# Kernel optimization log

Measured on AMD Instinct MI355X. Metric: run time of the kernel, lower is better.

The kernel has to match this reference:

```python
import jax, jax.numpy as jnp
import numpy as np

B, S, HID = 1, 2048, 2048
H, KVH, D, VD = 32, 8, 128, 128
R = 64  # rope_dim = head_dim * partial_rotary_factor, rounded down to even
N_REP = H // KVH
SCALE = D ** -0.5
NEG = -1e9


def _rotate_half(x):
    half = x.shape[-1] // 2
    return jnp.concatenate([-x[..., half:], x[..., :half]], axis=-1)


def setup_inputs() -> dict:
    key = jax.random.key(0)
    ks = jax.random.split(key, 8)
    hidden_states = jax.random.normal(ks[0], (B, S, HID), dtype=jnp.float32)
    # RoPE angles: standard inverse-frequency positional embedding of width R
    inv_freq = 1.0 / (10000.0 ** (np.arange(0, R, 2, dtype=np.float32) / R))
    pos = np.arange(S, dtype=np.float32)
    freqs = np.outer(pos, inv_freq)                       # [S, R/2]
    emb = np.concatenate([freqs, freqs], axis=-1)         # [S, R]
    cos = jnp.asarray(np.cos(emb))[None].repeat(B, axis=0)  # [B, S, R]
    sin = jnp.asarray(np.sin(emb))[None].repeat(B, axis=0)
    # additive causal mask [B, 1, S, S]
    causal = jnp.triu(jnp.full((S, S), NEG, dtype=jnp.float32), k=1)
    attention_mask = jnp.broadcast_to(causal[None, None], (B, 1, S, S))
    std = 0.02
    Wq = jax.random.normal(ks[1], (H * D, HID), dtype=jnp.float32) * std
    Wk = jax.random.normal(ks[2], (KVH * D, HID), dtype=jnp.float32) * std
    Wv = jax.random.normal(ks[3], (KVH * VD, HID), dtype=jnp.float32) * std
    Wo = jax.random.normal(ks[4], (HID, H * VD), dtype=jnp.float32) * std
    sink_bias = jax.random.normal(ks[5], (H,), dtype=jnp.float32) * 0.5
    return {"hidden_states": hidden_states, "cos": cos, "sin": sin,
            "attention_mask": attention_mask, "Wq": Wq, "Wk": Wk, "Wv": Wv,
            "Wo": Wo, "sink_bias": sink_bias}


def reference(hidden_states, cos, sin, attention_mask, Wq, Wk, Wv, Wo, sink_bias):
    b, s, _ = hidden_states.shape
    # projections -> [B, heads, S, dim]
    q = (hidden_states @ Wq.T).reshape(b, s, H, D).transpose(0, 2, 1, 3)
    k = (hidden_states @ Wk.T).reshape(b, s, KVH, D).transpose(0, 2, 1, 3)
    v = (hidden_states @ Wv.T).reshape(b, s, KVH, VD).transpose(0, 2, 1, 3)
    # partial RoPE on first R dims
    c = cos[:, None, :, :]  # [B,1,S,R]
    si = sin[:, None, :, :]
    q_r, q_n = q[..., :R], q[..., R:]
    k_r, k_n = k[..., :R], k[..., R:]
    q = jnp.concatenate([q_r * c + _rotate_half(q_r) * si, q_n], axis=-1)
    k = jnp.concatenate([k_r * c + _rotate_half(k_r) * si, k_n], axis=-1)
    # GQA: repeat kv heads
    k_rep = jnp.repeat(k, N_REP, axis=1)
    v_rep = jnp.repeat(v, N_REP, axis=1)
    scores = jnp.einsum('bhqd,bhkd->bhqk', q, k_rep) * SCALE + attention_mask
    # extra attention-sink logit column per head
    sinks = jnp.broadcast_to(sink_bias.reshape(1, H, 1, 1), (b, H, s, 1))
    aw = jnp.concatenate([scores, sinks], axis=-1)            # [B,H,S,S+1]
    probs = jax.nn.softmax(aw, axis=-1)[..., :-1]             # drop sink column
    out = jnp.einsum('bhqk,bhkd->bhqd', probs, v_rep)
    out = out.transpose(0, 2, 1, 3).reshape(b, s, H * VD)
    return out @ Wo.T
```

## Files before the change

kernel.cpp:

```cpp
#include <hip/hip_runtime.h>

typedef unsigned short u16;
typedef unsigned int   u32;
typedef __bf16  bf16x8 __attribute__((ext_vector_type(8)));
typedef float   f32x4  __attribute__((ext_vector_type(4)));
typedef u16     u16x4  __attribute__((ext_vector_type(4)));
typedef u16     u16x8  __attribute__((ext_vector_type(8)));

#define S_LEN 2048
#define NH 32
#define NKVH 8
#define HD 128
#define QKVST 6144
#define AOST  4096
#define ATT_SCALE 0.08838834764831845f
#define RESCALE_THR 8.0f

__device__ __forceinline__ u16 f2bf(float f){
  u32 u = __builtin_bit_cast(u32, f);
  u += 0x7FFFu + ((u >> 16) & 1u);
  return (u16)(u >> 16);
}
__device__ __forceinline__ float bf2f(u16 h){
  u32 u = ((u32)h) << 16;
  return __builtin_bit_cast(float, u);
}
__device__ __forceinline__ void gload_lds16(const u16* g, u16* l){
  __builtin_amdgcn_global_load_lds(
      (const __attribute__((address_space(1))) void*)g,
      (__attribute__((address_space(3))) void*)l, 16, 0, 0);
}

__global__ void cvt_kernel(const f32x4* __restrict__ in, u16x4* __restrict__ out, int n4){
  int i = blockIdx.x * 256 + threadIdx.x;
  if (i >= n4) return;
  f32x4 v = in[i];
  u16x4 o;
  o[0] = f2bf(v[0]); o[1] = f2bf(v[1]); o[2] = f2bf(v[2]); o[3] = f2bf(v[3]);
  out[i] = o;
}

template<int OUT_BF16, int ROPE>
__global__ __launch_bounds__(256, 2)
void gemm_bt_kernel(const u16* __restrict__ X, const u16* __restrict__ W,
                    void* __restrict__ Cv, int M, int N, int K,
                    const float* __restrict__ cosv, const float* __restrict__ sinv){
  __shared__ __align__(16) u16 As[2][2][128 * 32];
  __shared__ __align__(16) u16 Bs[2][2][128 * 32];
  const int m0 = blockIdx.y * 128, n0 = blockIdx.x * 128;
  const int tid = threadIdx.x;
  const int wave = tid >> 6, lane = tid & 63;
  const int wm = wave >> 1, wn = wave & 1;
  const int g = lane >> 4, ln = lane & 15;
  const int r0 = tid >> 2;
  const int cc = (tid & 3) * 8;
  f32x4 acc[4][4] = {};
  const u16* xa0 = X + (size_t)(m0 + r0) * K + cc;
  const u16* xa1 = X + (size_t)(m0 + r0 + 64) * K + cc;
  const u16* wb0 = W + (size_t)(n0 + r0) * K + cc;
  const u16* wb1 = W + (size_t)(n0 + r0 + 64) * K + cc;

  auto stage = [&](int buf, int k0){
    #pragma unroll
    for (int s = 0; s < 2; s++){
      const int kc = k0 + s * 32;
      gload_lds16(xa0 + kc, &As[buf][s][tid * 8]);
      gload_lds16(xa1 + kc, &As[buf][s][2048 + tid * 8]);
      gload_lds16(wb0 + kc, &Bs[buf][s][tid * 8]);
      gload_lds16(wb1 + kc, &Bs[buf][s][2048 + tid * 8]);
    }
  };

  stage(0, 0);
  __syncthreads();
  int cur = 0;
  for (int k0 = 0; k0 < K; k0 += 64){
    if (k0 + 64 < K) stage(cur ^ 1, k0 + 64);
    #pragma unroll
    for (int s = 0; s < 2; s++){
      bf16x8 a[4], b[4];
      #pragma unroll
      for (int f = 0; f < 4; f++) a[f] = *(const bf16x8*)&As[cur][s][(wm * 64 + f * 16 + ln) * 32 + g * 8];
      #pragma unroll
      for (int f = 0; f < 4; f++) b[f] = *(const bf16x8*)&Bs[cur][s][(wn * 64 + f * 16 + ln) * 32 + g * 8];
      __builtin_amdgcn_s_setprio(1);
      #pragma unroll
      for (int i = 0; i < 4; i++)
        #pragma unroll
        for (int j = 0; j < 4; j++)
          acc[i][j] = __builtin_amdgcn_mfma_f32_16x16x32_bf16(a[i], b[j], acc[i][j], 0, 0, 0);
      __builtin_amdgcn_s_setprio(0);
    }
    __syncthreads();
    cur ^= 1;
  }
  if (ROPE && wn == 0 && n0 < 5120){
    #pragma unroll
    for (int i = 0; i < 4; i++)
      #pragma unroll
      for (int r = 0; r < 4; r++){
        const int row = m0 + wm * 64 + i * 16 + g * 4 + r;
        #pragma unroll
        for (int j = 0; j < 2; j++){
          const int d = j * 16 + ln;
          float c  = cosv[row * 64 + d];
          float sn = sinv[row * 64 + d];
          float x0 = acc[i][j][r], x1 = acc[i][j + 2][r];
          acc[i][j][r]     = x0 * c - x1 * sn;
          acc[i][j + 2][r] = x1 * c + x0 * sn;
        }
      }
  }
  #pragma unroll
  for (int i = 0; i < 4; i++)
    #pragma unroll
    for (int j = 0; j < 4; j++)
      #pragma unroll
      for (int r = 0; r < 4; r++){
        int row = m0 + wm * 64 + i * 16 + g * 4 + r;
        int col = n0 + wn * 64 + j * 16 + ln;
        if (OUT_BF16) ((u16*)Cv)[(size_t)row * N + col] = f2bf(acc[i][j][r]);
        else          ((float*)Cv)[(size_t)row * N + col] = acc[i][j][r];
      }
}

__global__ void vtrans_kernel(const u16* __restrict__ QKV, u16* __restrict__ VT){
  int idx = blockIdx.x * 256 + threadIdx.x;
  if (idx >= NKVH * HD * S_LEN) return;
  int s   = idx & (S_LEN - 1);
  int vd  = (idx >> 11) & (HD - 1);
  int kvh = idx >> 18;
  VT[idx] = QKV[(size_t)s * QKVST + 5120 + kvh * HD + vd];
}

__global__ __launch_bounds__(256, 2)
void attn_kernel(const u16* __restrict__ QKV, const u16* __restrict__ VT,
                 const float* __restrict__ sinkb, u16* __restrict__ AO){
  __shared__ __align__(16) u16 Ks[2][64 * 128];
  __shared__ __align__(16) u16 Vs[2][144 * 64];
  __shared__ __align__(16) u16 Ps[4][16 * 64];
  const int b   = blockIdx.x;
  const int kvh = b & 7;
  const int h   = kvh * 4 + ((b >> 3) & 3);
  const int qt  = 31 - (b >> 5);
  const int tid = threadIdx.x;
  const int w = tid >> 6, lane = tid & 63;
  const int g = lane >> 4, ln = lane & 15;
  const int q0 = qt * 64;
  const int qw = q0 + w * 16;

  const u16* Kbase = QKV + 4096 + kvh * HD;
  const u16* Vbase = VT + (size_t)kvh * HD * S_LEN;

  auto stage = [&](int buf, int kt){
    const int k0 = kt * 64;
    #pragma unroll
    for (int p = 0; p < 4; p++){
      int idx = p * 256 + tid;
      int r = idx >> 4, c16 = idx & 15;
      gload_lds16(Kbase + (size_t)(k0 + r) * QKVST + ((c16 ^ (r & 7)) * 8), &Ks[buf][idx * 8]);
    }
    #pragma unroll
    for (int p = 0; p < 4; p++){
      int idx = p * 256 + tid;
      int vd = idx >> 3, c8 = idx & 7;
      gload_lds16(Vbase + (size_t)vd * S_LEN + k0 + ((c8 ^ (vd & 7)) * 8), &Vs[buf][idx * 8]);
    }
  };

  for (int i = tid; i < 16 * 64; i += 256){
    u16 v = (i < 64) ? (u16)0x3F80 : (u16)0;
    Vs[0][128 * 64 + i] = v;
    Vs[1][128 * 64 + i] = v;
  }

  bf16x8 qf[4];
  const u16* qrow = QKV + (size_t)(qw + ln) * QKVST + h * HD;
  #pragma unroll
  for (int t = 0; t < 4; t++) qf[t] = *(const bf16x8*)(qrow + t * 32 + g * 8);

  f32x4 O[9] = {};
  float m_r[4];
  #pragma unroll
  for (int r = 0; r < 4; r++) m_r[r] = -3.0e38f;

  const int nkt = qt + 1;
  stage(0, 0);
  __syncthreads();
  int cur = 0;

  for (int kt = 0; kt < nkt; kt++){
    const int k0 = kt * 64;
    if (kt + 1 < nkt) stage(cur ^ 1, kt + 1);

    const u16* Kc = Ks[cur];
    f32x4 sc[4] = {};
    __builtin_amdgcn_s_setprio(1);
    #pragma unroll
    for (int f = 0; f < 4; f++){
      const int krow = f * 16 + ln;
      #pragma unroll
      for (int t = 0; t < 4; t++){
        bf16x8 kf = *(const bf16x8*)&Kc[krow * 128 + ((t * 32 + g * 8) ^ ((ln & 7) << 3))];
        sc[f] = __builtin_amdgcn_mfma_f32_16x16x32_bf16(qf[t], kf, sc[f], 0, 0, 0);
      }
    }
    __builtin_amdgcn_s_setprio(0);

    const bool diag = (kt == qt);
    float pv[4][4];
    #pragma unroll
    for (int f = 0; f < 4; f++)
      #pragma unroll
      for (int r = 0; r < 4; r++){
        float v = sc[f][r] * ATT_SCALE;
        if (diag && (k0 + f * 16 + ln > qw + g * 4 + r)) v = -1e30f;
        pv[f][r] = v;
      }
    float mx[4];
    #pragma unroll
    for (int r = 0; r < 4; r++){
      float t = fmaxf(fmaxf(pv[0][r], pv[1][r]), fmaxf(pv[2][r], pv[3][r]));
      #pragma unroll
      for (int d = 1; d < 16; d <<= 1) t = fmaxf(t, __shfl_xor(t, d));
      mx[r] = t;
    }
    int ok = (mx[0] <= m_r[0] + RESCALE_THR) & (mx[1] <= m_r[1] + RESCALE_THR)
           & (mx[2] <= m_r[2] + RESCALE_THR) & (mx[3] <= m_r[3] + RESCALE_THR);
    if (!__all(ok)){
      float sf_[4];
      #pragma unroll
      for (int r = 0; r < 4; r++){
        float mn = fmaxf(m_r[r], mx[r]);
        sf_[r] = __expf(m_r[r] - mn);
        m_r[r] = mn;
      }
      #pragma unroll
      for (int fn = 0; fn < 9; fn++)
        #pragma unroll
        for (int r = 0; r < 4; r++) O[fn][r] *= sf_[r];
    }
    u16* Pw = Ps[w];
    #pragma unroll
    for (int r = 0; r < 4; r++){
      const int row = g * 4 + r;
      #pragma unroll
      for (int f = 0; f < 4; f++){
        float p = __expf(pv[f][r] - m_r[r]);
        Pw[row * 64 + ((f * 16 + ln) ^ ((row & 7) << 3))] = f2bf(p);
      }
    }
    const u16* Vc = Vs[cur];
    bf16x8 pa0 = *(const bf16x8*)&Pw[ln * 64 + ((g * 8)      ^ ((ln & 7) << 3))];
    bf16x8 pa1 = *(const bf16x8*)&Pw[ln * 64 + ((32 + g * 8) ^ ((ln & 7) << 3))];
    __builtin_amdgcn_s_setprio(1);
    #pragma unroll
    for (int fn = 0; fn < 9; fn++){
      const int vr = fn * 16 + ln;
      bf16x8 v0 = *(const bf16x8*)&Vc[vr * 64 + ((g * 8)      ^ ((ln & 7) << 3))];
      bf16x8 v1 = *(const bf16x8*)&Vc[vr * 64 + ((32 + g * 8) ^ ((ln & 7) << 3))];
      O[fn] = __builtin_amdgcn_mfma_f32_16x16x32_bf16(pa0, v0, O[fn], 0, 0, 0);
      O[fn] = __builtin_amdgcn_mfma_f32_16x16x32_bf16(pa1, v1, O[fn], 0, 0, 0);
    }
    __builtin_amdgcn_s_setprio(0);

    __syncthreads();
    cur ^= 1;
  }
  float sb = sinkb[h];
  #pragma unroll
  for (int r = 0; r < 4; r++){
    float l = __shfl(O[8][r], lane & 48);
    float mt = fmaxf(m_r[r], sb);
    float lt = l * __expf(m_r[r] - mt) + __expf(sb - mt);
    float osc = __expf(m_r[r] - mt) / lt;
    #pragma unroll
    for (int fn = 0; fn < 8; fn++)
      AO[(size_t)(qw + g * 4 + r) * AOST + h * HD + fn * 16 + ln] = f2bf(O[fn][r] * osc);
  }
}

extern "C" void kernel_launch(void* const* d_in, const int* in_sizes, int n_in,
                              void* d_out, int out_size, void* d_ws, size_t ws_size,
                              hipStream_t stream){
  (void)in_sizes; (void)n_in; (void)out_size; (void)ws_size;
  const float* hs    = (const float*)d_in[0];
  const float* cosv  = (const float*)d_in[1];
  const float* sinv  = (const float*)d_in[2];
  const float* Wq    = (const float*)d_in[4];
  const float* Wk    = (const float*)d_in[5];
  const float* Wv    = (const float*)d_in[6];
  const float* Wo    = (const float*)d_in[7];
  const float* sinkb = (const float*)d_in[8];
  float* out = (float*)d_out;

  char* ws = (char*)d_ws;
  u16* XB    = (u16*)(ws);
  u16* WQKVB = (u16*)(ws + 8388608);
  u16* WOB   = (u16*)(ws + 33554432);
  u16* QKV   = (u16*)(ws + 50331648);
  u16* VT    = (u16*)(ws + 75497472);
  u16* AO    = (u16*)(ws + 79691776);

  cvt_kernel<<<4096, 256, 0, stream>>>((const f32x4*)hs, (u16x4*)XB, 1048576);
  cvt_kernel<<<8192, 256, 0, stream>>>((const f32x4*)Wq, (u16x4*)WQKVB, 2097152);
  cvt_kernel<<<2048, 256, 0, stream>>>((const f32x4*)Wk, (u16x4*)(WQKVB + 4096 * 2048), 524288);
  cvt_kernel<<<2048, 256, 0, stream>>>((const f32x4*)Wv, (u16x4*)(WQKVB + 5120 * 2048), 524288);
  cvt_kernel<<<8192, 256, 0, stream>>>((const f32x4*)Wo, (u16x4*)WOB, 2097152);

  gemm_bt_kernel<1, 1><<<dim3(48, 16), 256, 0, stream>>>(XB, WQKVB, QKV, 2048, 6144, 2048, cosv, sinv);

  vtrans_kernel<<<8192, 256, 0, stream>>>(QKV, VT);

  attn_kernel<<<dim3(1024), 256, 0, stream>>>(QKV, VT, sinkb, AO);

  gemm_bt_kernel<0, 0><<<dim3(16, 16), 256, 0, stream>>>(AO, WOB, out, 2048, 2048, 4096, nullptr, nullptr);
}
```

Measured before the change: 259.3 us.

## Double attention Q tile per block and fold softmax scale into QKV GEMM

```diff
diff --git a/kernel.cpp b/kernel.cpp
--- a/kernel.cpp
+++ b/kernel.cpp
@@ -94,22 +94,32 @@
     __syncthreads();
     cur ^= 1;
   }
-  if (ROPE && wn == 0 && n0 < 5120){
-    #pragma unroll
-    for (int i = 0; i < 4; i++)
-      #pragma unroll
-      for (int r = 0; r < 4; r++){
-        const int row = m0 + wm * 64 + i * 16 + g * 4 + r;
-        #pragma unroll
-        for (int j = 0; j < 2; j++){
-          const int d = j * 16 + ln;
-          float c  = cosv[row * 64 + d];
-          float sn = sinv[row * 64 + d];
-          float x0 = acc[i][j][r], x1 = acc[i][j + 2][r];
-          acc[i][j][r]     = x0 * c - x1 * sn;
-          acc[i][j + 2][r] = x1 * c + x0 * sn;
-        }
-      }
+  if (ROPE){
+    if (wn == 0 && n0 < 5120){
+      #pragma unroll
+      for (int i = 0; i < 4; i++)
+        #pragma unroll
+        for (int r = 0; r < 4; r++){
+          const int row = m0 + wm * 64 + i * 16 + g * 4 + r;
+          #pragma unroll
+          for (int j = 0; j < 2; j++){
+            const int d = j * 16 + ln;
+            float c  = cosv[row * 64 + d];
+            float sn = sinv[row * 64 + d];
+            float x0 = acc[i][j][r], x1 = acc[i][j + 2][r];
+            acc[i][j][r]     = x0 * c - x1 * sn;
+            acc[i][j + 2][r] = x1 * c + x0 * sn;
+          }
+        }
+    }
+    if (n0 < 4096){
+      #pragma unroll
+      for (int i = 0; i < 4; i++)
+        #pragma unroll
+        for (int j = 0; j < 4; j++)
+          #pragma unroll
+          for (int r = 0; r < 4; r++) acc[i][j][r] *= ATT_SCALE;
+    }
   }
   #pragma unroll
   for (int i = 0; i < 4; i++)
@@ -137,17 +147,17 @@
 void attn_kernel(const u16* __restrict__ QKV, const u16* __restrict__ VT,
                  const float* __restrict__ sinkb, u16* __restrict__ AO){
   __shared__ __align__(16) u16 Ks[2][64 * 128];
-  __shared__ __align__(16) u16 Vs[2][144 * 64];
-  __shared__ __align__(16) u16 Ps[4][16 * 64];
+  __shared__ __align__(16) u16 Vs[2][128 * 64];
+  __shared__ __align__(16) u16 Ps[4][32 * 64];
   const int b   = blockIdx.x;
   const int kvh = b & 7;
   const int h   = kvh * 4 + ((b >> 3) & 3);
-  const int qt  = 31 - (b >> 5);
+  const int qt  = 15 - (b >> 5);
   const int tid = threadIdx.x;
   const int w = tid >> 6, lane = tid & 63;
   const int g = lane >> 4, ln = lane & 15;
-  const int q0 = qt * 64;
-  const int qw = q0 + w * 16;
+  const int q0 = qt * 128;
+  const int qw = q0 + w * 32;
 
   const u16* Kbase = QKV + 4096 + kvh * HD;
   const u16* Vbase = VT + (size_t)kvh * HD * S_LEN;
@@ -168,23 +178,28 @@
     }
   };
 
-  for (int i = tid; i < 16 * 64; i += 256){
-    u16 v = (i < 64) ? (u16)0x3F80 : (u16)0;
-    Vs[0][128 * 64 + i] = v;
-    Vs[1][128 * 64 + i] = v;
+  u16x8 ob;
+  #pragma unroll
+  for (int j = 0; j < 8; j++) ob[j] = (ln == 0) ? (u16)0x3F80 : (u16)0;
+  const bf16x8 onesf = __builtin_bit_cast(bf16x8, ob);
+
+  bf16x8 qf[2][4];
+  #pragma unroll
+  for (int qh = 0; qh < 2; qh++){
+    const u16* qrow = QKV + (size_t)(qw + qh * 16 + ln) * QKVST + h * HD;
+    #pragma unroll
+    for (int t = 0; t < 4; t++) qf[qh][t] = *(const bf16x8*)(qrow + t * 32 + g * 8);
   }
 
-  bf16x8 qf[4];
-  const u16* qrow = QKV + (size_t)(qw + ln) * QKVST + h * HD;
-  #pragma unroll
-  for (int t = 0; t < 4; t++) qf[t] = *(const bf16x8*)(qrow + t * 32 + g * 8);
-
-  f32x4 O[9] = {};
-  float m_r[4];
-  #pragma unroll
-  for (int r = 0; r < 4; r++) m_r[r] = -3.0e38f;
-
-  const int nkt = qt + 1;
+  f32x4 O[2][8] = {};
+  f32x4 L[2] = {};
+  float m_r[2][4];
+  #pragma unroll
+  for (int qh = 0; qh < 2; qh++)
+    #pragma unroll
+    for (int r = 0; r < 4; r++) m_r[qh][r] = -3.0e38f;
+
+  const int nkt = 2 * qt + 2;
   stage(0, 0);
   __syncthreads();
   int cur = 0;
@@ -193,91 +208,121 @@
     const int k0 = kt * 64;
     if (kt + 1 < nkt) stage(cur ^ 1, kt + 1);
 
-    const u16* Kc = Ks[cur];
-    f32x4 sc[4] = {};
-    __builtin_amdgcn_s_setprio(1);
-    #pragma unroll
-    for (int f = 0; f < 4; f++){
-      const int krow = f * 16 + ln;
-      #pragma unroll
-      for (int t = 0; t < 4; t++){
-        bf16x8 kf = *(const bf16x8*)&Kc[krow * 128 + ((t * 32 + g * 8) ^ ((ln & 7) << 3))];
-        sc[f] = __builtin_amdgcn_mfma_f32_16x16x32_bf16(qf[t], kf, sc[f], 0, 0, 0);
+    if (k0 < qw + 32){
+      const u16* Kc = Ks[cur];
+      f32x4 sc[2][4] = {};
+      __builtin_amdgcn_s_setprio(1);
+      #pragma unroll
+      for (int f = 0; f < 4; f++){
+        const int krow = f * 16 + ln;
+        #pragma unroll
+        for (int t = 0; t < 4; t++){
+          bf16x8 kf = *(const bf16x8*)&Kc[krow * 128 + ((t * 32 + g * 8) ^ ((ln & 7) << 3))];
+          sc[0][f] = __builtin_amdgcn_mfma_f32_16x16x32_bf16(qf[0][t], kf, sc[0][f], 0, 0, 0);
+          sc[1][f] = __builtin_amdgcn_mfma_f32_16x16x32_bf16(qf[1][t], kf, sc[1][f], 0, 0, 0);
+        }
       }
-    }
-    __builtin_amdgcn_s_setprio(0);
-
-    const bool diag = (kt == qt);
-    float pv[4][4];
-    #pragma unroll
-    for (int f = 0; f < 4; f++)
-      #pragma unroll
-      for (int r = 0; r < 4; r++){
-        float v = sc[f][r] * ATT_SCALE;
-        if (diag && (k0 + f * 16 + ln > qw + g * 4 + r)) v = -1e30f;
-        pv[f][r] = v;
+      __builtin_amdgcn_s_setprio(0);
+
+      const bool needmask = (k0 + 63 > qw);
+      float pv[2][4][4];
+      #pragma unroll
+      for (int qh = 0; qh < 2; qh++)
+        #pragma unroll
+        for (int f = 0; f < 4; f++)
+          #pragma unroll
+          for (int r = 0; r < 4; r++){
+            float v = sc[qh][f][r];
+            if (needmask && (k0 + f * 16 + ln > qw + qh * 16 + g * 4 + r)) v = -1e30f;
+            pv[qh][f][r] = v;
+          }
+      float mx[2][4];
+      #pragma unroll
+      for (int qh = 0; qh < 2; qh++)
+        #pragma unroll
+        for (int r = 0; r < 4; r++){
+          float t = fmaxf(fmaxf(pv[qh][0][r], pv[qh][1][r]), fmaxf(pv[qh][2][r], pv[qh][3][r]));
+          #pragma unroll
+          for (int d = 1; d < 16; d <<= 1) t = fmaxf(t, __shfl_xor(t, d));
+          mx[qh][r] = t;
+        }
+      int ok = 1;
+      #pragma unroll
+      for (int qh = 0; qh < 2; qh++)
+        #pragma unroll
+        for (int r = 0; r < 4; r++) ok &= (mx[qh][r] <= m_r[qh][r] + RESCALE_THR);
+      if (!__all(ok)){
+        #pragma unroll
+        for (int qh = 0; qh < 2; qh++){
+          float sf_[4];
+          #pragma unroll
+          for (int r = 0; r < 4; r++){
+            float mn = fmaxf(m_r[qh][r], mx[qh][r]);
+            sf_[r] = __expf(m_r[qh][r] - mn);
+            m_r[qh][r] = mn;
+          }
+          #pragma unroll
+          for (int fn = 0; fn < 8; fn++)
+            #pragma unroll
+            for (int r = 0; r < 4; r++) O[qh][fn][r] *= sf_[r];
+          #pragma unroll
+          for (int r = 0; r < 4; r++) L[qh][r] *= sf_[r];
+        }
       }
-    float mx[4];
-    #pragma unroll
-    for (int r = 0; r < 4; r++){
-      float t = fmaxf(fmaxf(pv[0][r], pv[1][r]), fmaxf(pv[2][r], pv[3][r]));
-      #pragma unroll
-      for (int d = 1; d < 16; d <<= 1) t = fmaxf(t, __shfl_xor(t, d));
-      mx[r] = t;
-    }
-    int ok = (mx[0] <= m_r[0] + RESCALE_THR) & (mx[1] <= m_r[1] + RESCALE_THR)
-           & (mx[2] <= m_r[2] + RESCALE_THR) & (mx[3] <= m_r[3] + RESCALE_THR);
-    if (!__all(ok)){
-      float sf_[4];
-      #pragma unroll
-      for (int r = 0; r < 4; r++){
-        float mn = fmaxf(m_r[r], mx[r]);
-        sf_[r] = __expf(m_r[r] - mn);
-        m_r[r] = mn;
+      u16* Pw = Ps[w];
+      #pragma unroll
+      for (int qh = 0; qh < 2; qh++)
+        #pragma unroll
+        for (int r = 0; r < 4; r++){
+          const int row = qh * 16 + g * 4 + r;
+          #pragma unroll
+          for (int f = 0; f < 4; f++){
+            float p = __expf(pv[qh][f][r] - m_r[qh][r]);
+            Pw[row * 64 + ((f * 16 + ln) ^ ((row & 7) << 3))] = f2bf(p);
+          }
+        }
+      const u16* Vc = Vs[cur];
+      bf16x8 pa[2][2];
+      #pragma unroll
+      for (int qh = 0; qh < 2; qh++)
+        #pragma unroll
+        for (int hf = 0; hf < 2; hf++)
+          pa[qh][hf] = *(const bf16x8*)&Pw[(qh * 16 + ln) * 64 + ((hf * 32 + g * 8) ^ ((ln & 7) << 3))];
+      __builtin_amdgcn_s_setprio(1);
+      #pragma unroll
+      for (int fn = 0; fn < 8; fn++){
+        const int vr = fn * 16 + ln;
+        #pragma unroll
+        for (int hf = 0; hf < 2; hf++){
+          bf16x8 vf = *(const bf16x8*)&Vc[vr * 64 + ((hf * 32 + g * 8) ^ ((ln & 7) << 3))];
+          O[0][fn] = __builtin_amdgcn_mfma_f32_16x16x32_bf16(pa[0][hf], vf, O[0][fn], 0, 0, 0);
+          O[1][fn] = __builtin_amdgcn_mfma_f32_16x16x32_bf16(pa[1][hf], vf, O[1][fn], 0, 0, 0);
+        }
       }
       #pragma unroll
-      for (int fn = 0; fn < 9; fn++)
-        #pragma unroll
-        for (int r = 0; r < 4; r++) O[fn][r] *= sf_[r];
-    }
-    u16* Pw = Ps[w];
-    #pragma unroll
-    for (int r = 0; r < 4; r++){
-      const int row = g * 4 + r;
-      #pragma unroll
-      for (int f = 0; f < 4; f++){
-        float p = __expf(pv[f][r] - m_r[r]);
-        Pw[row * 64 + ((f * 16 + ln) ^ ((row & 7) << 3))] = f2bf(p);
-      }
-    }
-    const u16* Vc = Vs[cur];
-    bf16x8 pa0 = *(const bf16x8*)&Pw[ln * 64 + ((g * 8)      ^ ((ln & 7) << 3))];
-    bf16x8 pa1 = *(const bf16x8*)&Pw[ln * 64 + ((32 + g * 8) ^ ((ln & 7) << 3))];
-    __builtin_amdgcn_s_setprio(1);
-    #pragma unroll
-    for (int fn = 0; fn < 9; fn++){
-      const int vr = fn * 16 + ln;
-      bf16x8 v0 = *(const bf16x8*)&Vc[vr * 64 + ((g * 8)      ^ ((ln & 7) << 3))];
-      bf16x8 v1 = *(const bf16x8*)&Vc[vr * 64 + ((32 + g * 8) ^ ((ln & 7) << 3))];
-      O[fn] = __builtin_amdgcn_mfma_f32_16x16x32_bf16(pa0, v0, O[fn], 0, 0, 0);
-      O[fn] = __builtin_amdgcn_mfma_f32_16x16x32_bf16(pa1, v1, O[fn], 0, 0, 0);
-    }
-    __builtin_amdgcn_s_setprio(0);
+      for (int qh = 0; qh < 2; qh++)
+        #pragma unroll
+        for (int hf = 0; hf < 2; hf++)
+          L[qh] = __builtin_amdgcn_mfma_f32_16x16x32_bf16(pa[qh][hf], onesf, L[qh], 0, 0, 0);
+      __builtin_amdgcn_s_setprio(0);
+    }
 
     __syncthreads();
     cur ^= 1;
   }
   float sb = sinkb[h];
   #pragma unroll
-  for (int r = 0; r < 4; r++){
-    float l = __shfl(O[8][r], lane & 48);
-    float mt = fmaxf(m_r[r], sb);
-    float lt = l * __expf(m_r[r] - mt) + __expf(sb - mt);
-    float osc = __expf(m_r[r] - mt) / lt;
-    #pragma unroll
-    for (int fn = 0; fn < 8; fn++)
-      AO[(size_t)(qw + g * 4 + r) * AOST + h * HD + fn * 16 + ln] = f2bf(O[fn][r] * osc);
-  }
+  for (int qh = 0; qh < 2; qh++)
+    #pragma unroll
+    for (int r = 0; r < 4; r++){
+      float l = __shfl(L[qh][r], lane & 48);
+      float mt = fmaxf(m_r[qh][r], sb);
+      float lt = l * __expf(m_r[qh][r] - mt) + __expf(sb - mt);
+      float osc = __expf(m_r[qh][r] - mt) / lt;
+      #pragma unroll
+      for (int fn = 0; fn < 8; fn++)
+        AO[(size_t)(qw + qh * 16 + g * 4 + r) * AOST + h * HD + fn * 16 + ln] = f2bf(O[qh][fn][r] * osc);
+    }
 }
 
 extern "C" void kernel_launch(void* const* d_in, const int* in_sizes, int n_in,
@@ -312,7 +357,7 @@
 
   vtrans_kernel<<<8192, 256, 0, stream>>>(QKV, VT);
 
-  attn_kernel<<<dim3(1024), 256, 0, stream>>>(QKV, VT, sinkb, AO);
+  attn_kernel<<<dim3(512), 256, 0, stream>>>(QKV, VT, sinkb, AO);
 
   gemm_bt_kernel<0, 0><<<dim3(16, 16), 256, 0, stream>>>(AO, WOB, out, 2048, 2048, 4096, nullptr, nullptr);
 }
```

After: 285.3 us. 1.1x slower.
